# Optimization experiments

Measured on AMD Instinct MI355X. Metric: run time of the kernel, lower is better.

## Reference

```python
import jax, jax.numpy as jnp
import numpy as np

DIM = 256
HEADS = 8
DH = 32            # dim_head
CT, CH, CW = 4, 8, 8  # cuboid_size
G = 8              # global tokens
INNER = HEADS * DH
SCALE = DH ** -0.5


def setup_inputs() -> dict:
    key = jax.random.key(0)
    k0, k1, k2, k3 = jax.random.split(key, 4)
    x = jax.random.normal(k0, (2, 8, 64, 64, DIM), jnp.float32)
    Wqkv = jax.random.normal(k1, (DIM, 3 * INNER), jnp.float32) * 0.02
    Wout = jax.random.normal(k2, (INNER, DIM), jnp.float32) * 0.02
    bout = jnp.zeros((DIM,), jnp.float32)
    gtok = jax.random.normal(k3, (1, G, DIM), jnp.float32)
    return {"x": x, "Wqkv": Wqkv, "Wout": Wout, "bout": bout, "gtok": gtok}


def reference(x, Wqkv, Wout, bout, gtok):
    b, t, h, w, d = x.shape
    pad_t = (-t) % CT
    pad_h = (-h) % CH
    pad_w = (-w) % CW
    # F.pad(..., mode='replicate') on trailing spatial dims == edge padding
    xp = jnp.pad(x, ((0, 0), (0, pad_t), (0, pad_h), (0, pad_w), (0, 0)), mode="edge")
    nt, nh, nw = xp.shape[1], xp.shape[2], xp.shape[3]
    Tn, Hn, Wn = nt // CT, nh // CH, nw // CW
    # partition into cuboid windows: (b*Tn*Hn*Wn, CT*CH*CW, d)
    xc = xp.reshape(b, Tn, CT, Hn, CH, Wn, CW, d)
    xc = xc.transpose(0, 1, 3, 5, 2, 4, 6, 7).reshape(b * Tn * Hn * Wn, CT * CH * CW, d)
    nB = xc.shape[0]
    # prepend shared global tokens
    g = jnp.broadcast_to(gtok, (nB, G, d))
    xc = jnp.concatenate([g, xc], axis=1)  # (nB, G + cuboid_len, d)
    # qkv projection and head split
    qkv = xc @ Wqkv
    q, k, v = jnp.split(qkv, 3, axis=-1)

    def to_heads(z):  # (nB, n, INNER) -> (nB, HEADS, n, DH)
        return z.reshape(nB, z.shape[1], HEADS, DH).transpose(0, 2, 1, 3)

    q, k, v = to_heads(q), to_heads(k), to_heads(v)
    attn = jax.nn.softmax(jnp.einsum("bhid,bhjd->bhij", q, k) * SCALE, axis=-1)
    o = jnp.einsum("bhij,bhjd->bhid", attn, v)
    o = o.transpose(0, 2, 1, 3).reshape(nB, -1, INNER)
    o = o @ Wout + bout
    o = o[:, G:, :]  # drop global tokens
    # un-partition back to (b, nt, nh, nw, d)
    o = o.reshape(b, Tn, Hn, Wn, CT, CH, CW, d)
    o = o.transpose(0, 1, 4, 2, 5, 3, 6, 7).reshape(b, nt, nh, nw, d)
    return o[:, :t, :h, :w, :]
```

## Files before the change

kernel.cpp:

```cpp
#include <hip/hip_runtime.h>
#include <math.h>

typedef short short8 __attribute__((ext_vector_type(8)));
typedef float f32x4 __attribute__((ext_vector_type(4)));

static constexpr float SCALE = 0.17677669529663687f;

__device__ __forceinline__ ushort f2bf(float x) {
    uint u = __float_as_uint(x);
    u += 0x7fff + ((u >> 16) & 1);
    return (ushort)(u >> 16);
}

__device__ __forceinline__ const float* row_src(
    int bb, int tok, const float* __restrict__ x, const float* __restrict__ gt)
{
    if (tok < 8) return gt + tok * 256;
    int j = tok - 8;
    int wn = bb & 7, hn = (bb >> 3) & 7, tn = (bb >> 6) & 1, b = bb >> 7;
    int cw = j & 7, ch = (j >> 3) & 7, ct = j >> 6;
    return x + ((((size_t)(b * 8 + tn * 4 + ct)) * 64 + (hn * 8 + ch)) * 64
                + (wn * 8 + cw)) * 256;
}

union F8 { ushort4 q[2]; short8 v; };

__global__ __launch_bounds__(256)
void k_prep(const float* __restrict__ Wq, const float* __restrict__ Wo,
            ushort* __restrict__ WqtH, ushort* __restrict__ WotH)
{
    int i = blockIdx.x * 256 + threadIdx.x;
    if (i < 196608) {
        uint k = (uint)i / 768u, n = (uint)i - k * 768u;
        WqtH[n * 256 + k] = f2bf(Wq[i]);
    } else {
        int j = i - 196608;
        uint k = (uint)j >> 8, n = (uint)j & 255u;
        WotH[n * 256 + k] = f2bf(Wo[j]);
    }
}

__global__ __launch_bounds__(256)
void k_gath(const float* __restrict__ x, const float* __restrict__ gt,
            ushort* __restrict__ xg)
{
    int idx = blockIdx.x * 256 + threadIdx.x;
    int row = idx >> 5;
    int c = (idx & 31) * 8;
    int bb = row / 264, tok = row - bb * 264;
    const float* src = row_src(bb, tok, x, gt) + c;
    float4 a = *(const float4*)src;
    float4 b = *(const float4*)(src + 4);
    union { ushort4 u4[2]; int4 i4; } pk;
    pk.u4[0] = make_ushort4(f2bf(a.x), f2bf(a.y), f2bf(a.z), f2bf(a.w));
    pk.u4[1] = make_ushort4(f2bf(b.x), f2bf(b.y), f2bf(b.z), f2bf(b.w));
    *(int4*)(xg + (size_t)row * 256 + c) = pk.i4;
}

#define GP 36
__global__ __launch_bounds__(256, 4)
void k_qkv(const ushort* __restrict__ xg, const ushort* __restrict__ WtH,
           ushort* __restrict__ qkv, int nb, int bb0, int mrows)
{
    int g = blockIdx.x;
    int xcd = g & 7;
    int j6 = g >> 3;
    int m_t = (j6 / 6) * 8 + xcd;
    int n_t = j6 % 6;
    if (m_t >= nb) return;
    const int m0 = m_t * 128, n0 = n_t * 128;

    __shared__ ushort SM[2 * 128 * GP];
    ushort* Ah = SM;
    ushort* Bh = SM + 128 * GP;
    const int tid = threadIdx.x;
    const int lane = tid & 63, wid = tid >> 6;
    const int ln = lane & 15, lg = lane >> 4;
    const int wm = wid >> 1, wn = wid & 1;

    const int srow = tid >> 1;
    const int kh = (tid & 1) * 16;
    int mst = m0 + srow;
    if (mst >= mrows) mst = mrows - 1;
    const ushort* rsrc = xg + (size_t)mst * 256 + kh;
    const ushort* bsrcH = WtH + (size_t)(n0 + srow) * 256 + kh;

    f32x4 acc[4][4];
#pragma unroll
    for (int i = 0; i < 4; ++i)
#pragma unroll
        for (int j = 0; j < 4; ++j) acc[i][j] = (f32x4){0.f, 0.f, 0.f, 0.f};

    ushort4 aset[2][4], bset[2][4];
#pragma unroll
    for (int j = 0; j < 4; ++j) {
        aset[0][j] = *(const ushort4*)(rsrc + 4 * j);
        bset[0][j] = *(const ushort4*)(bsrcH + 4 * j);
        aset[1][j] = *(const ushort4*)(rsrc + 32 + 4 * j);
        bset[1][j] = *(const ushort4*)(bsrcH + 32 + 4 * j);
    }

#pragma unroll
    for (int it = 0; it < 8; ++it) {
        const int s = it & 1;
        __syncthreads();
#pragma unroll
        for (int j = 0; j < 4; ++j) {
            *(ushort4*)&Ah[srow * GP + kh + 4 * j] = aset[s][j];
            *(ushort4*)&Bh[srow * GP + kh + 4 * j] = bset[s][j];
        }
        __syncthreads();

        if (it + 2 < 8) {
            const int ktn = 32 * (it + 2);
#pragma unroll
            for (int j = 0; j < 4; ++j) {
                aset[s][j] = *(const ushort4*)(rsrc + ktn + 4 * j);
                bset[s][j] = *(const ushort4*)(bsrcH + ktn + 4 * j);
            }
        }

        short8 af[4], bf[4];
#pragma unroll
        for (int mi = 0; mi < 4; ++mi) {
            int base = (wm * 64 + mi * 16 + ln) * GP + 4 * lg;
            F8 t;
            t.q[0] = *(const ushort4*)&Ah[base]; t.q[1] = *(const ushort4*)&Ah[base + 16];
            af[mi] = t.v;
        }
#pragma unroll
        for (int ni = 0; ni < 4; ++ni) {
            int base = (wn * 64 + ni * 16 + ln) * GP + 4 * lg;
            F8 t;
            t.q[0] = *(const ushort4*)&Bh[base]; t.q[1] = *(const ushort4*)&Bh[base + 16];
            bf[ni] = t.v;
        }
#pragma unroll
        for (int mi = 0; mi < 4; ++mi)
#pragma unroll
            for (int ni = 0; ni < 4; ++ni)
                acc[mi][ni] = __builtin_amdgcn_mfma_f32_16x16x32_bf16(af[mi], bf[ni], acc[mi][ni], 0, 0, 0);
    }

    float* Tr = (float*)SM;
    const int trow = tid >> 3;
    const int t8 = (tid & 7) * 8;
#pragma unroll
    for (int mi = 0; mi < 4; ++mi) {
        __syncthreads();
#pragma unroll
        for (int ni = 0; ni < 4; ++ni)
#pragma unroll
            for (int r = 0; r < 4; ++r)
                Tr[(wm * 16 + lg * 4 + r) * 132 + wn * 64 + ni * 16 + ln] = acc[mi][ni][r];
        __syncthreads();
        int gm = m0 + (trow >> 4) * 64 + mi * 16 + (trow & 15);
        if (gm < mrows) {
            ushort* dst = qkv + (size_t)gm * 768 + n0;
            const float* src = &Tr[trow * 132];
#pragma unroll
            for (int half = 0; half < 2; ++half) {
                float4 a = *(const float4*)(src + half * 64 + t8);
                float4 b = *(const float4*)(src + half * 64 + t8 + 4);
                union { ushort4 u4[2]; int4 i4; } pk;
                pk.u4[0] = make_ushort4(f2bf(a.x), f2bf(a.y), f2bf(a.z), f2bf(a.w));
                pk.u4[1] = make_ushort4(f2bf(b.x), f2bf(b.y), f2bf(b.z), f2bf(b.w));
                *(int4*)(dst + half * 64 + t8) = pk.i4;
            }
        }
    }
}

#define KPAD 36
#define VPAD 296
__global__ __launch_bounds__(256, 4)
void k_attn(ushort* __restrict__ qkv)
{
    __shared__ ushort Khi[272 * KPAD];
    __shared__ ushort Vt[32 * VPAD];

    const int lb = blockIdx.x, h = blockIdx.y;
    const int tid = threadIdx.x;
    const int wid = tid >> 6;
    const int lane = tid & 63;
    const int ln = lane & 15, lg = lane >> 4;
    ushort* base = qkv + (size_t)lb * (264 * 768);
    const int koff = 256 + h * 32, voff = 512 + h * 32;

    for (int slot = tid; slot < 1056; slot += 256) {
        int rp = slot >> 3;
        int c4 = (slot & 7) * 4;
        int r0 = rp * 2;
        const ushort* p0 = base + (size_t)r0 * 768;
        const ushort* p1 = p0 + 768;
        ushort4 k0 = *(const ushort4*)(p0 + koff + c4);
        ushort4 k1 = *(const ushort4*)(p1 + koff + c4);
        ushort4 v0 = *(const ushort4*)(p0 + voff + c4);
        ushort4 v1 = *(const ushort4*)(p1 + voff + c4);
        *(ushort4*)&Khi[r0 * KPAD + c4] = k0;
        *(ushort4*)&Khi[(r0 + 1) * KPAD + c4] = k1;
        *(ushort2*)&Vt[(c4 + 0) * VPAD + r0] = make_ushort2(v0.x, v1.x);
        *(ushort2*)&Vt[(c4 + 1) * VPAD + r0] = make_ushort2(v0.y, v1.y);
        *(ushort2*)&Vt[(c4 + 2) * VPAD + r0] = make_ushort2(v0.z, v1.z);
        *(ushort2*)&Vt[(c4 + 3) * VPAD + r0] = make_ushort2(v0.w, v1.w);
    }
    for (int slot = tid; slot < 1024; slot += 256) {
        int d = slot >> 5;
        Vt[d * VPAD + 264 + (slot & 31)] = 0;
    }

    short8 qh[4];
#pragma unroll
    for (int t = 0; t < 4; ++t) {
        int qrow = 8 + (wid * 4 + t) * 16 + ln;
        const ushort* qp = base + (size_t)qrow * 768 + h * 32;
        F8 fh;
        fh.q[0] = *(const ushort4*)(qp + 4 * lg);
        fh.q[1] = *(const ushort4*)(qp + 16 + 4 * lg);
        qh[t] = fh.v;
    }

    f32x4 acc[4][2];
    float lsum[4];
#pragma unroll
    for (int t = 0; t < 4; ++t) {
        acc[t][0] = (f32x4){0.f, 0.f, 0.f, 0.f};
        acc[t][1] = (f32x4){0.f, 0.f, 0.f, 0.f};
        lsum[t] = 0.f;
    }

    __syncthreads();

    for (int g = 0; g < 8; ++g) {
        const int kt0 = g * 32;
        F8 fa;
        const ushort* pka = &Khi[(kt0 + ln) * KPAD + 4 * lg];
        fa.q[0] = *(const ushort4*)pka; fa.q[1] = *(const ushort4*)(pka + 16);
        short8 ka = fa.v;
        const ushort* pkb = &Khi[(kt0 + 16 + ln) * KPAD + 4 * lg];
        fa.q[0] = *(const ushort4*)pkb; fa.q[1] = *(const ushort4*)(pkb + 16);
        short8 kb = fa.v;
        const ushort* pv0 = &Vt[ln * VPAD + kt0 + 4 * lg];
        fa.q[0] = *(const ushort4*)pv0; fa.q[1] = *(const ushort4*)(pv0 + 16);
        short8 va = fa.v;
        const ushort* pv1 = &Vt[(16 + ln) * VPAD + kt0 + 4 * lg];
        fa.q[0] = *(const ushort4*)pv1; fa.q[1] = *(const ushort4*)(pv1 + 16);
        short8 vb = fa.v;

#pragma unroll
        for (int t = 0; t < 4; ++t) {
            f32x4 sa = {0.f, 0.f, 0.f, 0.f}, sb = {0.f, 0.f, 0.f, 0.f};
            sa = __builtin_amdgcn_mfma_f32_16x16x32_bf16(ka, qh[t], sa, 0, 0, 0);
            sb = __builtin_amdgcn_mfma_f32_16x16x32_bf16(kb, qh[t], sb, 0, 0, 0);
            float p[8];
#pragma unroll
            for (int c = 0; c < 4; ++c) {
                p[c] = __expf(sa[c] * SCALE);
                p[4 + c] = __expf(sb[c] * SCALE);
            }
            lsum[t] += ((p[0] + p[1]) + (p[2] + p[3])) + ((p[4] + p[5]) + (p[6] + p[7]));
            F8 pf;
            pf.q[0] = make_ushort4(f2bf(p[0]), f2bf(p[1]), f2bf(p[2]), f2bf(p[3]));
            pf.q[1] = make_ushort4(f2bf(p[4]), f2bf(p[5]), f2bf(p[6]), f2bf(p[7]));
            acc[t][0] = __builtin_amdgcn_mfma_f32_16x16x32_bf16(va, pf.v, acc[t][0], 0, 0, 0);
            acc[t][1] = __builtin_amdgcn_mfma_f32_16x16x32_bf16(vb, pf.v, acc[t][1], 0, 0, 0);
        }
    }

    {
        F8 fa;
        const ushort* pka = &Khi[(256 + ln) * KPAD + 4 * lg];
        fa.q[0] = *(const ushort4*)pka; fa.q[1] = *(const ushort4*)(pka + 16);
        short8 ka = fa.v;
        const ushort* pv0 = &Vt[ln * VPAD + 256 + 4 * lg];
        fa.q[0] = *(const ushort4*)pv0; fa.q[1] = *(const ushort4*)(pv0 + 16);
        short8 va = fa.v;
        const ushort* pv1 = &Vt[(16 + ln) * VPAD + 256 + 4 * lg];
        fa.q[0] = *(const ushort4*)pv1; fa.q[1] = *(const ushort4*)(pv1 + 16);
        short8 vb = fa.v;

#pragma unroll
        for (int t = 0; t < 4; ++t) {
            f32x4 sa = {0.f, 0.f, 0.f, 0.f};
            sa = __builtin_amdgcn_mfma_f32_16x16x32_bf16(ka, qh[t], sa, 0, 0, 0);
            float p[4];
#pragma unroll
            for (int c = 0; c < 4; ++c)
                p[c] = (lg >= 2) ? 0.f : __expf(sa[c] * SCALE);
            lsum[t] += (p[0] + p[1]) + (p[2] + p[3]);
            F8 pf;
            pf.q[0] = make_ushort4(f2bf(p[0]), f2bf(p[1]), f2bf(p[2]), f2bf(p[3]));
            pf.q[1] = make_ushort4(0, 0, 0, 0);
            acc[t][0] = __builtin_amdgcn_mfma_f32_16x16x32_bf16(va, pf.v, acc[t][0], 0, 0, 0);
            acc[t][1] = __builtin_amdgcn_mfma_f32_16x16x32_bf16(vb, pf.v, acc[t][1], 0, 0, 0);
        }
    }

#pragma unroll
    for (int t = 0; t < 4; ++t) {
        float l = lsum[t];
        l += __shfl_xor(l, 16);
        l += __shfl_xor(l, 32);
        float inv = 1.f / l;
        ushort* op = base + (size_t)(8 + (wid * 4 + t) * 16 + ln) * 768 + h * 32;
#pragma unroll
        for (int r = 0; r < 4; ++r) {
            op[lg * 4 + r] = f2bf(acc[t][0][r] * inv);
            op[16 + lg * 4 + r] = f2bf(acc[t][1][r] * inv);
        }
    }
}

__global__ __launch_bounds__(256, 4)
void k_out(const ushort* __restrict__ qkv, const ushort* __restrict__ WtH,
           const float* __restrict__ bias, float* __restrict__ out, int bb0)
{
    __shared__ ushort SM[2 * 128 * GP];
    ushort* Ah = SM;
    ushort* Bh = SM + 128 * GP;
    const int tid = threadIdx.x;
    const int lane = tid & 63, wid = tid >> 6;
    const int ln = lane & 15, lg = lane >> 4;
    const int wm = wid >> 1, wn = wid & 1;
    const int n0 = blockIdx.x * 128, m0 = blockIdx.y * 128;

    const int srow = tid >> 1;
    const int kh = (tid & 1) * 16;
    int mst = m0 + srow;
    int lb = mst >> 8, j0 = mst & 255;
    const ushort* rsrc = qkv + (size_t)(lb * 264 + 8 + j0) * 768;
    const ushort* bsrcH = WtH + (size_t)(n0 + srow) * 256 + kh;

    f32x4 acc[4][4];
#pragma unroll
    for (int i = 0; i < 4; ++i)
#pragma unroll
        for (int j = 0; j < 4; ++j) acc[i][j] = (f32x4){0.f, 0.f, 0.f, 0.f};

    ushort4 aset[2][4], bset[2][4];
#pragma unroll
    for (int j = 0; j < 4; ++j) {
        aset[0][j] = *(const ushort4*)(rsrc + kh + 4 * j);
        bset[0][j] = *(const ushort4*)(bsrcH + 4 * j);
        aset[1][j] = *(const ushort4*)(rsrc + kh + 32 + 4 * j);
        bset[1][j] = *(const ushort4*)(bsrcH + 32 + 4 * j);
    }

#pragma unroll
    for (int it = 0; it < 8; ++it) {
        const int s = it & 1;
        __syncthreads();
#pragma unroll
        for (int j = 0; j < 4; ++j) {
            *(ushort4*)&Ah[srow * GP + kh + 4 * j] = aset[s][j];
            *(ushort4*)&Bh[srow * GP + kh + 4 * j] = bset[s][j];
        }
        __syncthreads();

        if (it + 2 < 8) {
            const int ktn = 32 * (it + 2);
#pragma unroll
            for (int j = 0; j < 4; ++j) {
                aset[s][j] = *(const ushort4*)(rsrc + kh + ktn + 4 * j);
                bset[s][j] = *(const ushort4*)(bsrcH + ktn + 4 * j);
            }
        }

        short8 af[4], bf[4];
#pragma unroll
        for (int mi = 0; mi < 4; ++mi) {
            int base = (wm * 64 + mi * 16 + ln) * GP + 4 * lg;
            F8 t;
            t.q[0] = *(const ushort4*)&Ah[base]; t.q[1] = *(const ushort4*)&Ah[base + 16];
            af[mi] = t.v;
        }
#pragma unroll
        for (int ni = 0; ni < 4; ++ni) {
            int base = (wn * 64 + ni * 16 + ln) * GP + 4 * lg;
            F8 t;
            t.q[0] = *(const ushort4*)&Bh[base]; t.q[1] = *(const ushort4*)&Bh[base + 16];
            bf[ni] = t.v;
        }
#pragma unroll
        for (int mi = 0; mi < 4; ++mi)
#pragma unroll
            for (int ni = 0; ni < 4; ++ni)
                acc[mi][ni] = __builtin_amdgcn_mfma_f32_16x16x32_bf16(af[mi], bf[ni], acc[mi][ni], 0, 0, 0);
    }

    float bcol[4];
#pragma unroll
    for (int ni = 0; ni < 4; ++ni) bcol[ni] = bias[n0 + wn * 64 + ni * 16 + ln];

    float* Tr = (float*)SM;
    const int trow = tid >> 3;
    const int tc = (tid & 7) * 4;
#pragma unroll
    for (int mi = 0; mi < 4; ++mi) {
        __syncthreads();
#pragma unroll
        for (int ni = 0; ni < 4; ++ni)
#pragma unroll
            for (int r = 0; r < 4; ++r)
                Tr[(wm * 16 + lg * 4 + r) * 132 + wn * 64 + ni * 16 + ln] = acc[mi][ni][r] + bcol[ni];
        __syncthreads();
        int m = m0 + (trow >> 4) * 64 + mi * 16 + (trow & 15);
        int lb2 = m >> 8, j = m & 255;
        int bb = bb0 + lb2;
        int wn2 = bb & 7, hn = (bb >> 3) & 7, tn = (bb >> 6) & 1, b = bb >> 7;
        int cw = j & 7, ch = (j >> 3) & 7, ct = j >> 6;
        float* dst = out + ((((size_t)(b * 8 + tn * 4 + ct)) * 64 + (hn * 8 + ch)) * 64
                            + (wn2 * 8 + cw)) * 256 + n0;
        const float* src = &Tr[trow * 132];
#pragma unroll
        for (int jj = 0; jj < 4; ++jj)
            *(float4*)(dst + tc + 32 * jj) = *(const float4*)(src + tc + 32 * jj);
    }
}

extern "C" void kernel_launch(void* const* d_in, const int* in_sizes, int n_in,
                              void* d_out, int out_size, void* d_ws, size_t ws_size,
                              hipStream_t stream) {
    const float* x    = (const float*)d_in[0];
    const float* Wqkv = (const float*)d_in[1];
    const float* Wout = (const float*)d_in[2];
    const float* bout = (const float*)d_in[3];
    const float* gtok = (const float*)d_in[4];
    float* out = (float*)d_out;

    ushort* WqtH = (ushort*)d_ws;
    ushort* WotH = WqtH + 196608;
    ushort* xg   = (ushort*)((char*)d_ws + 1048576);
    ushort* qkv  = xg + (size_t)67584 * 256;

    k_prep<<<1024, 256, 0, stream>>>(Wqkv, Wout, WqtH, WotH);
    k_gath<<<8448, 256, 0, stream>>>(x, gtok, xg);

    const size_t head = 1048576 + (size_t)67584 * 256 * 2;
    const size_t per_block = (size_t)264 * 768 * 2;
    int P = (int)((ws_size - head) / per_block);
    if (P > 256) P = 256;
    if (P < 1) P = 1;

    for (int bb0 = 0; bb0 < 256; bb0 += P) {
        int pb = (256 - bb0 < P) ? (256 - bb0) : P;
        int mrows = pb * 264;
        int nb = (mrows + 127) / 128;
        int grid1 = 8 * (((nb + 7) / 8) * 6);
        k_qkv<<<dim3(grid1), 256, 0, stream>>>(xg + (size_t)bb0 * 264 * 256, WqtH, qkv, nb, bb0, mrows);
        k_attn<<<dim3(pb, 8), 256, 0, stream>>>(qkv);
        k_out<<<dim3(2, pb * 2), 256, 0, stream>>>(qkv, WotH, bout, out, bb0);
    }
}
```

Before: 145.7 us.

## Fuse cuboid gather and bf16 conversion into QKV GEMM loads

Removes the separate gather kernel that wrote a bf16 copy of the partitioned input, and has the QKV GEMM read fp32 rows straight from x (or the global tokens) and convert to bf16 in registers. The prefetch loads are also split so global loads go into temporaries before the MFMA loop and are committed after it, which lets load latency overlap compute in both GEMMs. This saves one full read and write pass over the activations and a kernel launch. In exchange the QKV GEMM reads twice as many bytes per A tile, and the same x rows are re-read and re-converted by each of the six N tiles.

```diff
diff --git a/kernel.cpp b/kernel.cpp
--- a/kernel.cpp
+++ b/kernel.cpp
@@ -10,6 +10,9 @@
     uint u = __float_as_uint(x);
     u += 0x7fff + ((u >> 16) & 1);
     return (ushort)(u >> 16);
+}
+__device__ __forceinline__ ushort4 cvt4(float4 v) {
+    return make_ushort4(f2bf(v.x), f2bf(v.y), f2bf(v.z), f2bf(v.w));
 }
 
 __device__ __forceinline__ const float* row_src(
@@ -40,27 +43,11 @@
     }
 }
 
-__global__ __launch_bounds__(256)
-void k_gath(const float* __restrict__ x, const float* __restrict__ gt,
-            ushort* __restrict__ xg)
-{
-    int idx = blockIdx.x * 256 + threadIdx.x;
-    int row = idx >> 5;
-    int c = (idx & 31) * 8;
-    int bb = row / 264, tok = row - bb * 264;
-    const float* src = row_src(bb, tok, x, gt) + c;
-    float4 a = *(const float4*)src;
-    float4 b = *(const float4*)(src + 4);
-    union { ushort4 u4[2]; int4 i4; } pk;
-    pk.u4[0] = make_ushort4(f2bf(a.x), f2bf(a.y), f2bf(a.z), f2bf(a.w));
-    pk.u4[1] = make_ushort4(f2bf(b.x), f2bf(b.y), f2bf(b.z), f2bf(b.w));
-    *(int4*)(xg + (size_t)row * 256 + c) = pk.i4;
-}
-
 #define GP 36
 __global__ __launch_bounds__(256, 4)
-void k_qkv(const ushort* __restrict__ xg, const ushort* __restrict__ WtH,
-           ushort* __restrict__ qkv, int nb, int bb0, int mrows)
+void k_qkv(const float* __restrict__ x, const ushort* __restrict__ WtH,
+           const float* __restrict__ gt, ushort* __restrict__ qkv,
+           int nb, int bb0, int mrows)
 {
     int g = blockIdx.x;
     int xcd = g & 7;
@@ -82,7 +69,8 @@
     const int kh = (tid & 1) * 16;
     int mst = m0 + srow;
     if (mst >= mrows) mst = mrows - 1;
-    const ushort* rsrc = xg + (size_t)mst * 256 + kh;
+    int lb = mst / 264, tok = mst - lb * 264;
+    const float* rsrc = row_src(bb0 + lb, tok, x, gt) + kh;
     const ushort* bsrcH = WtH + (size_t)(n0 + srow) * 256 + kh;
 
     f32x4 acc[4][4];
@@ -94,9 +82,9 @@
     ushort4 aset[2][4], bset[2][4];
 #pragma unroll
     for (int j = 0; j < 4; ++j) {
-        aset[0][j] = *(const ushort4*)(rsrc + 4 * j);
+        aset[0][j] = cvt4(*(const float4*)(rsrc + 4 * j));
         bset[0][j] = *(const ushort4*)(bsrcH + 4 * j);
-        aset[1][j] = *(const ushort4*)(rsrc + 32 + 4 * j);
+        aset[1][j] = cvt4(*(const float4*)(rsrc + 32 + 4 * j));
         bset[1][j] = *(const ushort4*)(bsrcH + 32 + 4 * j);
     }
 
@@ -111,12 +99,15 @@
         }
         __syncthreads();
 
-        if (it + 2 < 8) {
+        float4 ta[4];
+        ushort4 tb[4];
+        const bool more = (it + 2 < 8);
+        if (more) {
             const int ktn = 32 * (it + 2);
 #pragma unroll
             for (int j = 0; j < 4; ++j) {
-                aset[s][j] = *(const ushort4*)(rsrc + ktn + 4 * j);
-                bset[s][j] = *(const ushort4*)(bsrcH + ktn + 4 * j);
+                ta[j] = *(const float4*)(rsrc + ktn + 4 * j);
+                tb[j] = *(const ushort4*)(bsrcH + ktn + 4 * j);
             }
         }
 
@@ -140,6 +131,14 @@
 #pragma unroll
             for (int ni = 0; ni < 4; ++ni)
                 acc[mi][ni] = __builtin_amdgcn_mfma_f32_16x16x32_bf16(af[mi], bf[ni], acc[mi][ni], 0, 0, 0);
+
+        if (more) {
+#pragma unroll
+            for (int j = 0; j < 4; ++j) {
+                aset[s][j] = cvt4(ta[j]);
+                bset[s][j] = tb[j];
+            }
+        }
     }
 
     float* Tr = (float*)SM;
@@ -163,8 +162,8 @@
                 float4 a = *(const float4*)(src + half * 64 + t8);
                 float4 b = *(const float4*)(src + half * 64 + t8 + 4);
                 union { ushort4 u4[2]; int4 i4; } pk;
-                pk.u4[0] = make_ushort4(f2bf(a.x), f2bf(a.y), f2bf(a.z), f2bf(a.w));
-                pk.u4[1] = make_ushort4(f2bf(b.x), f2bf(b.y), f2bf(b.z), f2bf(b.w));
+                pk.u4[0] = cvt4(a);
+                pk.u4[1] = cvt4(b);
                 *(int4*)(dst + half * 64 + t8) = pk.i4;
             }
         }
@@ -328,7 +327,7 @@
     const int kh = (tid & 1) * 16;
     int mst = m0 + srow;
     int lb = mst >> 8, j0 = mst & 255;
-    const ushort* rsrc = qkv + (size_t)(lb * 264 + 8 + j0) * 768;
+    const ushort* rsrc = qkv + (size_t)(lb * 264 + 8 + j0) * 768 + kh;
     const ushort* bsrcH = WtH + (size_t)(n0 + srow) * 256 + kh;
 
     f32x4 acc[4][4];
@@ -340,9 +339,9 @@
     ushort4 aset[2][4], bset[2][4];
 #pragma unroll
     for (int j = 0; j < 4; ++j) {
-        aset[0][j] = *(const ushort4*)(rsrc + kh + 4 * j);
+        aset[0][j] = *(const ushort4*)(rsrc + 4 * j);
         bset[0][j] = *(const ushort4*)(bsrcH + 4 * j);
-        aset[1][j] = *(const ushort4*)(rsrc + kh + 32 + 4 * j);
+        aset[1][j] = *(const ushort4*)(rsrc + 32 + 4 * j);
         bset[1][j] = *(const ushort4*)(bsrcH + 32 + 4 * j);
     }
 
@@ -357,12 +356,14 @@
         }
         __syncthreads();
 
-        if (it + 2 < 8) {
+        ushort4 ta[4], tb[4];
+        const bool more = (it + 2 < 8);
+        if (more) {
             const int ktn = 32 * (it + 2);
 #pragma unroll
             for (int j = 0; j < 4; ++j) {
-                aset[s][j] = *(const ushort4*)(rsrc + kh + ktn + 4 * j);
-                bset[s][j] = *(const ushort4*)(bsrcH + ktn + 4 * j);
+                ta[j] = *(const ushort4*)(rsrc + ktn + 4 * j);
+                tb[j] = *(const ushort4*)(bsrcH + ktn + 4 * j);
             }
         }
 
@@ -386,6 +387,14 @@
 #pragma unroll
             for (int ni = 0; ni < 4; ++ni)
                 acc[mi][ni] = __builtin_amdgcn_mfma_f32_16x16x32_bf16(af[mi], bf[ni], acc[mi][ni], 0, 0, 0);
+
+        if (more) {
+#pragma unroll
+            for (int j = 0; j < 4; ++j) {
+                aset[s][j] = ta[j];
+                bset[s][j] = tb[j];
+            }
+        }
     }
 
     float bcol[4];
@@ -430,15 +439,12 @@
 
     ushort* WqtH = (ushort*)d_ws;
     ushort* WotH = WqtH + 196608;
-    ushort* xg   = (ushort*)((char*)d_ws + 1048576);
-    ushort* qkv  = xg + (size_t)67584 * 256;
+    ushort* qkv = (ushort*)((char*)d_ws + 1048576);
 
     k_prep<<<1024, 256, 0, stream>>>(Wqkv, Wout, WqtH, WotH);
-    k_gath<<<8448, 256, 0, stream>>>(x, gtok, xg);
-
-    const size_t head = 1048576 + (size_t)67584 * 256 * 2;
+
     const size_t per_block = (size_t)264 * 768 * 2;
-    int P = (int)((ws_size - head) / per_block);
+    int P = (int)((ws_size - 1048576) / per_block);
     if (P > 256) P = 256;
     if (P < 1) P = 1;
 
@@ -447,7 +453,7 @@
         int mrows = pb * 264;
         int nb = (mrows + 127) / 128;
         int grid1 = 8 * (((nb + 7) / 8) * 6);
-        k_qkv<<<dim3(grid1), 256, 0, stream>>>(xg + (size_t)bb0 * 264 * 256, WqtH, qkv, nb, bb0, mrows);
+        k_qkv<<<dim3(grid1), 256, 0, stream>>>(x, WqtH, gtok, qkv, nb, bb0, mrows);
         k_attn<<<dim3(pb, 8), 256, 0, stream>>>(qkv);
         k_out<<<dim3(2, pb * 2), 256, 0, stream>>>(qkv, WotH, bout, out, bb0);
     }
```

After: 140.5 us. 3.5% less time.
